# Kernel tuning notes

Measured on AMD Instinct MI355X. Metric: run time of the kernel, lower is better.

The kernel has to match this reference:

```python
import jax, jax.numpy as jnp
import numpy as np

E = 1024  # embed_dim
NH = 16   # num_heads
HH, WW = 128, 128


def setup_inputs() -> dict:
    key = jax.random.key(0)
    ks = jax.random.split(key, 9)
    s = 0.02
    x = jax.random.normal(ks[0], (1, HH, WW, E), dtype=jnp.float32)
    d = {"x": x}
    for i, name in enumerate(["q", "k", "v", "o"]):
        d[f"W{name}"] = jax.random.normal(ks[1 + 2 * i], (E, E), dtype=jnp.float32) * s
        d[f"b{name}"] = jax.random.normal(ks[2 + 2 * i], (E,), dtype=jnp.float32) * s
    return d


def reference(x, Wq, bq, Wk, bk, Wv, bv, Wo, bo):
    B, h, w, e = x.shape
    D = e // NH  # head dim
    # projections + ReLU feature map on q, k (torch Linear: x @ W.T + b)
    q = jnp.maximum(x @ Wq.T + bq, 0.0).reshape(B, h, w, NH, D)
    k = jnp.maximum(x @ Wk.T + bk, 0.0).reshape(B, h, w, NH, D)
    v = (x @ Wv.T + bv).reshape(B, h, w, NH, D)
    # width-axis linear retention: kv state per (row h, head n)
    kv_w = jnp.einsum('bhwnd,bhwne->bhnde', k, v)        # [B,h,NH,D,D]
    out = jnp.einsum('bhwnd,bhnde->bhwne', q, kv_w)      # [B,h,w,NH,D]
    # height-axis linear retention: kv state per (col w, head n)
    kv_h = jnp.einsum('bhwnd,bhwne->bwnde', k, v)        # [B,w,NH,D,D]
    out = jnp.einsum('bhwne,bwnef->bhwnf', out, kv_h)    # [B,h,w,NH,D]
    out = out.reshape(B, h, w, e) @ Wo.T + bo
    return out.reshape(B, h * w, e)
```

## Files before the change

### kernel.cpp

```cpp
#include <hip/hip_runtime.h>
#include <hip/hip_bf16.h>
#include <stdint.h>


typedef __attribute__((ext_vector_type(4))) float floatx4;
typedef __attribute__((ext_vector_type(8))) short shortx8;

static __device__ __forceinline__ float bf2f(unsigned short h) {
  return __uint_as_float(((unsigned int)h) << 16);
}
static __device__ __forceinline__ unsigned short f2bf(float f) {
  unsigned int u = __float_as_uint(f);
  u += 0x7fffu + ((u >> 16) & 1u);
  return (unsigned short)(u >> 16);
}

static __device__ __forceinline__ void gload16(const void* g, void* l) {
  __builtin_amdgcn_global_load_lds(
      (const __attribute__((address_space(1))) void*)g,
      (__attribute__((address_space(3))) void*)l, 16, 0, 0);
}

__global__ __launch_bounds__(256) void cvt_all(
    const float* __restrict__ x, const float* __restrict__ Wq,
    const float* __restrict__ Wk, const float* __restrict__ Wv,
    const float* __restrict__ Wo, unsigned short* __restrict__ xb,
    unsigned short* __restrict__ wqkvb, unsigned short* __restrict__ wob) {
  const int b = blockIdx.x;
  const float* src;
  unsigned short* dst;
  int off;
  if (b < 16384) {
    src = x; dst = xb; off = b;
  } else if (b < 17408) {
    src = Wq; dst = wqkvb; off = b - 16384;
  } else if (b < 18432) {
    src = Wk; dst = wqkvb + 1048576; off = b - 17408;
  } else if (b < 19456) {
    src = Wv; dst = wqkvb + 2097152; off = b - 18432;
  } else {
    src = Wo; dst = wob; off = b - 19456;
  }
  const int i = (off * 256 + threadIdx.x) * 4;
  float4 f = *(const float4*)(src + i);
  ushort4 o;
  o.x = f2bf(f.x); o.y = f2bf(f.y); o.z = f2bf(f.z); o.w = f2bf(f.w);
  *(ushort4*)(dst + i) = o;
}

template <int MODE>
__global__ __launch_bounds__(256) void gemm_bt(
    const unsigned short* __restrict__ A,
    const unsigned short* __restrict__ BT,
    const float* __restrict__ b0, const float* __restrict__ b1,
    const float* __restrict__ b2,
    unsigned short* __restrict__ Oq, unsigned short* __restrict__ Ok,
    unsigned short* __restrict__ Ov, float* __restrict__ Of) {
  __shared__ __align__(16) unsigned short smem[18432];
  unsigned short* lA = smem;
  unsigned short* lB = smem + 4096;
  const int K = 1024;
  const int t = threadIdx.x;
  const int m0 = blockIdx.x * 128;
  const int n0 = blockIdx.y * 128;
  const int lane = t & 63;
  const int wv = t >> 6;
  const int wm = (wv & 1) * 64;
  const int wn = (wv >> 1) * 64;
  const int mrow = lane & 15;
  const int quad = lane >> 4;
  const int slot = quad ^ ((mrow >> 1) & 3);

  const int srow = t >> 2;
  const int scol = (((t & 3) ^ ((srow >> 1) & 3))) * 8;
  const unsigned short* gA0 = A + (size_t)(m0 + srow) * K + scol;
  const unsigned short* gA1 = A + (size_t)(m0 + 64 + srow) * K + scol;
  const unsigned short* gB0 = BT + (size_t)(n0 + srow) * K + scol;
  const unsigned short* gB1 = BT + (size_t)(n0 + 64 + srow) * K + scol;
  unsigned short* lA0 = &lA[t * 8];
  unsigned short* lA1 = &lA[2048 + t * 8];
  unsigned short* lB0 = &lB[t * 8];
  unsigned short* lB1 = &lB[2048 + t * 8];

  floatx4 acc[4][4] = {};
  for (int kk = 0; kk < K; kk += 32) {
    gload16(gA0 + kk, lA0);
    gload16(gA1 + kk, lA1);
    gload16(gB0 + kk, lB0);
    gload16(gB1 + kk, lB1);
    __syncthreads();
    shortx8 af[4], bfr[4];
#pragma unroll
    for (int i = 0; i < 4; ++i)
      af[i] = *(const shortx8*)&lA[(wm + i * 16 + mrow) * 32 + slot * 8];
#pragma unroll
    for (int j = 0; j < 4; ++j)
      bfr[j] = *(const shortx8*)&lB[(wn + j * 16 + mrow) * 32 + slot * 8];
#pragma unroll
    for (int i = 0; i < 4; ++i)
#pragma unroll
      for (int j = 0; j < 4; ++j)
        acc[i][j] = __builtin_amdgcn_mfma_f32_16x16x32_bf16(af[i], bfr[j],
                                                            acc[i][j], 0, 0, 0);
    __syncthreads();
  }

  if (MODE == 0) {
    const int sel = n0 >> 10;
    const float* bb = (sel == 0) ? b0 : ((sel == 1) ? b1 : b2);
    unsigned short* O = (sel == 0) ? Oq : ((sel == 1) ? Ok : Ov);
    const int nb = n0 & 1023;
    unsigned short* we = smem + wv * 4608;
#pragma unroll
    for (int j = 0; j < 4; ++j) {
      const int coll = j * 16 + mrow;
      const float bias = bb[nb + wn + coll];
#pragma unroll
      for (int i = 0; i < 4; ++i) {
#pragma unroll
        for (int r = 0; r < 4; ++r) {
          const int rowl = i * 16 + quad * 4 + r;
          float v = acc[i][j][r] + bias;
          if (sel < 2) v = fmaxf(v, 0.0f);
          we[rowl * 72 + coll] = f2bf(v);
        }
      }
    }
    __syncthreads();
    const int r8 = lane >> 3;
    const int c8 = lane & 7;
#pragma unroll
    for (int p = 0; p < 8; ++p) {
      const int rowl = r8 + p * 8;
      uint4 v = *(const uint4*)&we[rowl * 72 + c8 * 8];
      *(uint4*)&O[(size_t)(m0 + wm + rowl) * 1024 + nb + wn + c8 * 8] = v;
    }
  } else {
#pragma unroll
    for (int j = 0; j < 4; ++j) {
      const int col = n0 + wn + j * 16 + mrow;
      const float bias = b0[col];
#pragma unroll
      for (int i = 0; i < 4; ++i) {
#pragma unroll
        for (int r = 0; r < 4; ++r) {
          const int m = m0 + wm + i * 16 + quad * 4 + r;
          Of[(size_t)m * 1024 + col] = acc[i][j][r] + bias;
        }
      }
    }
  }
}

__global__ __launch_bounds__(256) void retention_fused(
    const unsigned short* __restrict__ S, const unsigned short* __restrict__ Kb,
    const unsigned short* __restrict__ Vb, unsigned short* __restrict__ D,
    int axis) {
  const int outer = blockIdx.x;
  const int n = blockIdx.y;
  __shared__ unsigned short lS[128 * 72];
  __shared__ unsigned short lKT[64 * 136];
  __shared__ unsigned short lVT[64 * 136];
  __shared__ unsigned short lKV[64 * 72];
  const int t = threadIdx.x;
  const size_t base = (axis == 0) ? ((size_t)outer << 17) : ((size_t)outer << 10);
  const size_t istr = (axis == 0) ? (size_t)1024 : (size_t)131072;
  const size_t nof = (size_t)(n << 6);

#pragma unroll
  for (int it = 0; it < 4; ++it) {
    const int r = it * 32 + (t >> 3);
    const int c = (t & 7) * 8;
    uint4 v = *(const uint4*)&S[base + (size_t)r * istr + nof + c];
    *(uint4*)&lS[r * 72 + c] = v;
  }
#pragma unroll
  for (int it = 0; it < 4; ++it) {
    const int w = it * 32 + (t & 31);
    const int d0 = (t >> 5) * 8;
    const size_t g = base + (size_t)w * istr + nof + d0;
    uint4 k4 = *(const uint4*)&Kb[g];
    uint4 v4 = *(const uint4*)&Vb[g];
    const unsigned short* kp = (const unsigned short*)&k4;
    const unsigned short* vp = (const unsigned short*)&v4;
#pragma unroll
    for (int i = 0; i < 8; ++i) {
      lKT[(d0 + i) * 136 + w] = kp[i];
      lVT[(d0 + i) * 136 + w] = vp[i];
    }
  }
  __syncthreads();

  const int lane = t & 63;
  const int wv = t >> 6;
  const int mrow = lane & 15;
  const int quad = lane >> 4;

  floatx4 acc1[4] = {};
#pragma unroll
  for (int ks = 0; ks < 4; ++ks) {
    shortx8 a = *(const shortx8*)&lVT[(wv * 16 + mrow) * 136 + ks * 32 + quad * 8];
#pragma unroll
    for (int j = 0; j < 4; ++j) {
      shortx8 b = *(const shortx8*)&lKT[(j * 16 + mrow) * 136 + ks * 32 + quad * 8];
      acc1[j] = __builtin_amdgcn_mfma_f32_16x16x32_bf16(a, b, acc1[j], 0, 0, 0);
    }
  }
#pragma unroll
  for (int j = 0; j < 4; ++j)
#pragma unroll
    for (int r = 0; r < 4; ++r)
      lKV[(wv * 16 + quad * 4 + r) * 72 + j * 16 + mrow] = f2bf(acc1[j][r]);
  __syncthreads();

  floatx4 acc2[2][4] = {};
#pragma unroll
  for (int ks = 0; ks < 2; ++ks) {
    shortx8 a2[2], b2[4];
#pragma unroll
    for (int i = 0; i < 2; ++i)
      a2[i] = *(const shortx8*)&lS[(wv * 32 + i * 16 + mrow) * 72 + ks * 32 + quad * 8];
#pragma unroll
    for (int j = 0; j < 4; ++j)
      b2[j] = *(const shortx8*)&lKV[(j * 16 + mrow) * 72 + ks * 32 + quad * 8];
#pragma unroll
    for (int i = 0; i < 2; ++i)
#pragma unroll
      for (int j = 0; j < 4; ++j)
        acc2[i][j] = __builtin_amdgcn_mfma_f32_16x16x32_bf16(a2[i], b2[j],
                                                             acc2[i][j], 0, 0, 0);
  }
#pragma unroll
  for (int i = 0; i < 2; ++i)
#pragma unroll
    for (int j = 0; j < 4; ++j)
#pragma unroll
      for (int r = 0; r < 4; ++r) {
        const int row = wv * 32 + i * 16 + quad * 4 + r;
        const int col = j * 16 + mrow;
        D[base + (size_t)row * istr + nof + col] = f2bf(acc2[i][j][r]);
      }
}

extern "C" void kernel_launch(void* const* d_in, const int* in_sizes, int n_in,
                              void* d_out, int out_size, void* d_ws, size_t ws_size,
                              hipStream_t stream) {
  const float* x  = (const float*)d_in[0];
  const float* Wq = (const float*)d_in[1];
  const float* bq = (const float*)d_in[2];
  const float* Wk = (const float*)d_in[3];
  const float* bk = (const float*)d_in[4];
  const float* Wv = (const float*)d_in[5];
  const float* bv = (const float*)d_in[6];
  const float* Wo = (const float*)d_in[7];
  const float* bo = (const float*)d_in[8];
  float* out = (float*)d_out;

  char* ws = (char*)d_ws;
  unsigned short* xb    = (unsigned short*)(ws + 0);
  unsigned short* wqkvb = (unsigned short*)(ws + 33554432);
  unsigned short* wob   = (unsigned short*)(ws + 39845888);
  unsigned short* qb    = (unsigned short*)(ws + 41943040);
  unsigned short* kb    = (unsigned short*)(ws + 75497472);
  unsigned short* vb    = (unsigned short*)(ws + 109051904);
  unsigned short* out1  = xb;
  unsigned short* out2  = qb;

  cvt_all<<<dim3(20480), dim3(256), 0, stream>>>(x, Wq, Wk, Wv, Wo, xb, wqkvb, wob);
  gemm_bt<0><<<dim3(128, 24), dim3(256), 0, stream>>>(
      xb, wqkvb, bq, bk, bv, qb, kb, vb, (float*)nullptr);
  retention_fused<<<dim3(128, 16), dim3(256), 0, stream>>>(qb, kb, vb, out1, 0);
  retention_fused<<<dim3(128, 16), dim3(256), 0, stream>>>(out1, kb, vb, out2, 1);
  gemm_bt<1><<<dim3(128, 8), dim3(256), 0, stream>>>(
      out2, wob, bo, nullptr, nullptr, nullptr, nullptr, nullptr, out);
}
```

Baseline: 354.8 us.

## Double-buffer A tile in LDS, load B fragments directly to registers, stage epilogue via LDS

The GEMM main loop now double-buffers the A tile in LDS with a prefetch of the next 32-wide k-slice. B fragments are loaded straight from global memory into registers, ping-ponging between two register sets, and the loop handles 64 k per iteration. The fp32 output epilogue is staged through LDS so rows can be written as coalesced float4 stores, and the bf16 epilogue now runs in two rounds so it needs only half the shared buffer. The retention kernel reuses the lVT buffer for the KV tile behind an extra barrier, cutting LDS use to allow more occupancy. In exchange, B loads are no longer shared through LDS, which raises global/L2 traffic per wave, and the epilogue gains extra barriers.

```diff
diff --git a/kernel.cpp b/kernel.cpp
--- a/kernel.cpp
+++ b/kernel.cpp
@@ -56,9 +56,8 @@
     const float* __restrict__ b2,
     unsigned short* __restrict__ Oq, unsigned short* __restrict__ Ok,
     unsigned short* __restrict__ Ov, float* __restrict__ Of) {
-  __shared__ __align__(16) unsigned short smem[18432];
+  __shared__ __align__(16) unsigned short smem[(MODE == 0) ? 9216 : 17408];
   unsigned short* lA = smem;
-  unsigned short* lB = smem + 4096;
   const int K = 1024;
   const int t = threadIdx.x;
   const int m0 = blockIdx.x * 128;
@@ -75,79 +74,132 @@
   const int scol = (((t & 3) ^ ((srow >> 1) & 3))) * 8;
   const unsigned short* gA0 = A + (size_t)(m0 + srow) * K + scol;
   const unsigned short* gA1 = A + (size_t)(m0 + 64 + srow) * K + scol;
-  const unsigned short* gB0 = BT + (size_t)(n0 + srow) * K + scol;
-  const unsigned short* gB1 = BT + (size_t)(n0 + 64 + srow) * K + scol;
-  unsigned short* lA0 = &lA[t * 8];
-  unsigned short* lA1 = &lA[2048 + t * 8];
-  unsigned short* lB0 = &lB[t * 8];
-  unsigned short* lB1 = &lB[2048 + t * 8];
+
+  const unsigned short* gB[4];
+#pragma unroll
+  for (int j = 0; j < 4; ++j)
+    gB[j] = BT + (size_t)(n0 + wn + j * 16 + mrow) * K + quad * 8;
 
   floatx4 acc[4][4] = {};
-  for (int kk = 0; kk < K; kk += 32) {
-    gload16(gA0 + kk, lA0);
-    gload16(gA1 + kk, lA1);
-    gload16(gB0 + kk, lB0);
-    gload16(gB1 + kk, lB1);
+  shortx8 bA[4], bB[4];
+
+  gload16(gA0, lA + t * 8);
+  gload16(gA1, lA + 2048 + t * 8);
+#pragma unroll
+  for (int j = 0; j < 4; ++j) bA[j] = *(const shortx8*)(gB[j]);
+
+  for (int kk = 0; kk < K; kk += 64) {
     __syncthreads();
-    shortx8 af[4], bfr[4];
-#pragma unroll
-    for (int i = 0; i < 4; ++i)
-      af[i] = *(const shortx8*)&lA[(wm + i * 16 + mrow) * 32 + slot * 8];
-#pragma unroll
-    for (int j = 0; j < 4; ++j)
-      bfr[j] = *(const shortx8*)&lB[(wn + j * 16 + mrow) * 32 + slot * 8];
-#pragma unroll
-    for (int i = 0; i < 4; ++i)
-#pragma unroll
-      for (int j = 0; j < 4; ++j)
-        acc[i][j] = __builtin_amdgcn_mfma_f32_16x16x32_bf16(af[i], bfr[j],
-                                                            acc[i][j], 0, 0, 0);
+    gload16(gA0 + kk + 32, lA + 4096 + t * 8);
+    gload16(gA1 + kk + 32, lA + 4096 + 2048 + t * 8);
+    {
+      shortx8 af[4];
+#pragma unroll
+      for (int i = 0; i < 4; ++i)
+        af[i] = *(const shortx8*)&lA[(wm + i * 16 + mrow) * 32 + slot * 8];
+#pragma unroll
+      for (int j = 0; j < 4; ++j) bB[j] = *(const shortx8*)(gB[j] + kk + 32);
+#pragma unroll
+      for (int i = 0; i < 4; ++i)
+#pragma unroll
+        for (int j = 0; j < 4; ++j)
+          acc[i][j] = __builtin_amdgcn_mfma_f32_16x16x32_bf16(af[i], bA[j],
+                                                              acc[i][j], 0, 0, 0);
+    }
     __syncthreads();
-  }
+    const bool pf = (kk + 64) < K;
+    if (pf) {
+      gload16(gA0 + kk + 64, lA + t * 8);
+      gload16(gA1 + kk + 64, lA + 2048 + t * 8);
+    }
+    {
+      shortx8 af[4];
+#pragma unroll
+      for (int i = 0; i < 4; ++i)
+        af[i] = *(const shortx8*)&lA[4096 + (wm + i * 16 + mrow) * 32 + slot * 8];
+      if (pf) {
+#pragma unroll
+        for (int j = 0; j < 4; ++j) bA[j] = *(const shortx8*)(gB[j] + kk + 64);
+      }
+#pragma unroll
+      for (int i = 0; i < 4; ++i)
+#pragma unroll
+        for (int j = 0; j < 4; ++j)
+          acc[i][j] = __builtin_amdgcn_mfma_f32_16x16x32_bf16(af[i], bB[j],
+                                                              acc[i][j], 0, 0, 0);
+    }
+  }
+  __syncthreads();
 
   if (MODE == 0) {
     const int sel = n0 >> 10;
     const float* bb = (sel == 0) ? b0 : ((sel == 1) ? b1 : b2);
     unsigned short* O = (sel == 0) ? Oq : ((sel == 1) ? Ok : Ov);
-    const int nb = n0 & 1023;
-    unsigned short* we = smem + wv * 4608;
-#pragma unroll
-    for (int j = 0; j < 4; ++j) {
-      const int coll = j * 16 + mrow;
-      const float bias = bb[nb + wn + coll];
-#pragma unroll
-      for (int i = 0; i < 4; ++i) {
-#pragma unroll
-        for (int r = 0; r < 4; ++r) {
-          const int rowl = i * 16 + quad * 4 + r;
-          float v = acc[i][j][r] + bias;
-          if (sel < 2) v = fmaxf(v, 0.0f);
-          we[rowl * 72 + coll] = f2bf(v);
-        }
-      }
-    }
-    __syncthreads();
+    const int nb2 = (n0 & 1023) + wn;
+    unsigned short* we = smem + (wv & 1) * 4608;
     const int r8 = lane >> 3;
     const int c8 = lane & 7;
 #pragma unroll
-    for (int p = 0; p < 8; ++p) {
-      const int rowl = r8 + p * 8;
-      uint4 v = *(const uint4*)&we[rowl * 72 + c8 * 8];
-      *(uint4*)&O[(size_t)(m0 + wm + rowl) * 1024 + nb + wn + c8 * 8] = v;
+    for (int round = 0; round < 2; ++round) {
+      if ((wv >> 1) == round) {
+#pragma unroll
+        for (int j = 0; j < 4; ++j) {
+          const int coll = j * 16 + mrow;
+          const float bias = bb[nb2 + coll];
+#pragma unroll
+          for (int i = 0; i < 4; ++i) {
+#pragma unroll
+            for (int r = 0; r < 4; ++r) {
+              float v = acc[i][j][r] + bias;
+              if (sel < 2) v = fmaxf(v, 0.0f);
+              we[(i * 16 + quad * 4 + r) * 72 + coll] = f2bf(v);
+            }
+          }
+        }
+      }
+      __syncthreads();
+      if ((wv >> 1) == round) {
+#pragma unroll
+        for (int p = 0; p < 8; ++p) {
+          const int rowl = r8 + p * 8;
+          uint4 v = *(const uint4*)&we[rowl * 72 + c8 * 8];
+          *(uint4*)&O[(size_t)(m0 + wm + rowl) * 1024 + nb2 + c8 * 8] = v;
+        }
+      }
+      __syncthreads();
     }
   } else {
-#pragma unroll
-    for (int j = 0; j < 4; ++j) {
-      const int col = n0 + wn + j * 16 + mrow;
-      const float bias = b0[col];
-#pragma unroll
-      for (int i = 0; i < 4; ++i) {
-#pragma unroll
-        for (int r = 0; r < 4; ++r) {
-          const int m = m0 + wm + i * 16 + quad * 4 + r;
-          Of[(size_t)m * 1024 + col] = acc[i][j][r] + bias;
+    float* we = (float*)smem + (wv & 1) * (64 * 68);
+    const int r8 = lane >> 3;
+    const int c8 = lane & 7;
+#pragma unroll
+    for (int round = 0; round < 2; ++round) {
+      if ((wv >> 1) == round) {
+#pragma unroll
+        for (int j = 0; j < 4; ++j) {
+          const int coll = j * 16 + mrow;
+          const float bias = b0[n0 + wn + coll];
+#pragma unroll
+          for (int i = 0; i < 4; ++i) {
+#pragma unroll
+            for (int r = 0; r < 4; ++r)
+              we[(i * 16 + quad * 4 + r) * 68 + coll] = acc[i][j][r] + bias;
+          }
         }
       }
+      __syncthreads();
+      if ((wv >> 1) == round) {
+#pragma unroll
+        for (int p = 0; p < 8; ++p) {
+          const int rowl = r8 + p * 8;
+          float4 v0 = *(const float4*)&we[rowl * 68 + c8 * 8];
+          float4 v1 = *(const float4*)&we[rowl * 68 + c8 * 8 + 4];
+          float* dst = Of + (size_t)(m0 + wm + rowl) * 1024 + n0 + wn + c8 * 8;
+          *(float4*)dst = v0;
+          *(float4*)(dst + 4) = v1;
+        }
+      }
+      __syncthreads();
     }
   }
 }
@@ -161,7 +213,7 @@
   __shared__ unsigned short lS[128 * 72];
   __shared__ unsigned short lKT[64 * 136];
   __shared__ unsigned short lVT[64 * 136];
-  __shared__ unsigned short lKV[64 * 72];
+  unsigned short* lKV = lVT;
   const int t = threadIdx.x;
   const size_t base = (axis == 0) ? ((size_t)outer << 17) : ((size_t)outer << 10);
   const size_t istr = (axis == 0) ? (size_t)1024 : (size_t)131072;
@@ -206,6 +258,7 @@
       acc1[j] = __builtin_amdgcn_mfma_f32_16x16x32_bf16(a, b, acc1[j], 0, 0, 0);
     }
   }
+  __syncthreads();
 #pragma unroll
   for (int j = 0; j < 4; ++j)
 #pragma unroll
```

Result: slower. 486.2 us (+37.0%).
